# Performance work log

Measured on AMD Instinct MI355X. Metric: run time of the kernel, lower is better.

Reference implementation:

```python
import jax, jax.numpy as jnp
import numpy as np

B = 16384          # batch size
NUM_NEG = 4
N = 1 + NUM_NEG    # items per row (pos + negs)
D = 128            # embedding_dim
F = 4              # num_factors
FS = D // F        # factor_size = 32
TD = 384           # bert_text_dim
NU = 100000        # num_users
NI = 100000        # num_items
HID = 150          # text MLP hidden
M = 2              # num_modalities


def _linear_init(k, fan_out, fan_in):
    bound = 1.0 / np.sqrt(fan_in)
    return jax.random.uniform(k, (fan_out, fan_in), jnp.float32, -bound, bound)


def setup_inputs() -> dict:
    key = jax.random.key(0)
    ks = jax.random.split(key, 12)
    batch = jax.random.randint(ks[0], (B, 1 + N), 0, NU)          # col0=user, cols1..5=items
    text = jax.random.normal(ks[1], (B, N, TD), dtype=jnp.float32)
    user_table = jax.random.normal(ks[2], (NU, D), dtype=jnp.float32)
    item_table = jax.random.normal(ks[3], (NI, D), dtype=jnp.float32)
    w1 = _linear_init(ks[4], HID, TD)
    b1 = jax.random.uniform(ks[5], (HID,), jnp.float32, -1/np.sqrt(TD), 1/np.sqrt(TD))
    w2 = _linear_init(ks[6], D, HID)
    b2 = jax.random.uniform(ks[7], (D,), jnp.float32, -1/np.sqrt(HID), 1/np.sqrt(HID))
    # per-factor attention MLPs, stacked over the F factors (all same size here)
    aw1 = jax.random.uniform(ks[8], (F, M, 3 * FS), jnp.float32, -1/np.sqrt(3*FS), 1/np.sqrt(3*FS))
    ab1 = jax.random.uniform(ks[9], (F, M), jnp.float32, -1/np.sqrt(3*FS), 1/np.sqrt(3*FS))
    aw2 = jax.random.uniform(ks[10], (F, M, M), jnp.float32, -1/np.sqrt(M), 1/np.sqrt(M))
    return dict(batch=batch, text=text, user_table=user_table, item_table=item_table,
                w1=w1, b1=b1, w2=w2, b2=b2, aw1=aw1, ab1=ab1, aw2=aw2)


def _leaky_relu(x):
    return jnp.where(x > 0, x, 0.01 * x)


def reference(batch, text, user_table, item_table, w1, b1, w2, b2, aw1, ab1, aw2):
    # text MLP: Linear -> LeakyReLU -> Linear -> LeakyReLU
    te = _leaky_relu(_leaky_relu(text @ w1.T + b1) @ w2.T + b2)   # [B,N,D]

    users = batch[:, 0]
    items = batch[:, 1:]
    u = user_table[users]                                          # [B,D]
    ie = item_table[items]                                         # [B,N,D]

    # split into F factors of size FS (vectorized over factor dim)
    uf = jnp.broadcast_to(u[:, None, :], ie.shape).reshape(B, N, F, FS)
    itf = ie.reshape(B, N, F, FS)
    tf = te.reshape(B, N, F, FS)

    cat = jnp.concatenate([uf, itf, tf], axis=-1)                  # [B,N,F,3*FS]
    nrm = jnp.linalg.norm(cat, axis=-1, keepdims=True)
    cat = cat / jnp.maximum(nrm, 1e-12)                            # F.normalize(dim=-1)

    h = jnp.tanh(jnp.einsum('bnfk,fmk->bnfm', cat, aw1) + ab1)     # [B,N,F,M]
    logits = jnp.einsum('bnfm,fom->bnfo', h, aw2)                  # [B,N,F,M]
    # torch nn.Softmax() with dim=None on a 3D tensor -> softmax over dim 0 (batch)
    attn = jax.nn.softmax(logits, axis=0)

    r_ui = attn[..., 0] * jax.nn.softplus(jnp.sum(uf * itf, axis=-1))  # [B,N,F]
    r_ut = attn[..., 1] * jax.nn.softplus(jnp.sum(uf * tf, axis=-1))   # [B,N,F]
    ratings = jnp.sum(r_ui + r_ut, axis=-1)                        # [B,N], sum over factors
    return ratings
```

## Files before the change

### kernel.cpp

```cpp
#include <hip/hip_runtime.h>
#include <hip/hip_bf16.h>

#define TDIM 384
#define HID 150
#define DD 128
#define ROWS 81920
#define RT 32

typedef __attribute__((ext_vector_type(8))) short short8;
typedef __attribute__((ext_vector_type(4))) float f32x4;

#define SMEM_BYTES 16896

__device__ __forceinline__ float lrelu(float x) { return x > 0.f ? x : 0.01f * x; }
__device__ __forceinline__ float softplusf(float x) {
    return fmaxf(x, 0.f) + log1pf(expf(-fabsf(x)));
}

__device__ __forceinline__ short8 pack8(const float4 a, const float4 b) {
    union { short8 s; __hip_bfloat16 h[8]; } u;
    u.h[0] = __float2bfloat16(a.x); u.h[1] = __float2bfloat16(a.y);
    u.h[2] = __float2bfloat16(a.z); u.h[3] = __float2bfloat16(a.w);
    u.h[4] = __float2bfloat16(b.x); u.h[5] = __float2bfloat16(b.y);
    u.h[6] = __float2bfloat16(b.z); u.h[7] = __float2bfloat16(b.w);
    return u.s;
}

__global__ __launch_bounds__(256)
void prep_w(const float* __restrict__ w1, const float* __restrict__ w2,
            short8* __restrict__ w1f, short8* __restrict__ w2f)
{
    const int idx = blockIdx.x * 256 + threadIdx.x;
    union { short8 s; __hip_bfloat16 h[8]; } u;
    if (idx < 7680) {
        const int kt = idx / 640, c = idx % 640;
        const int col = c >> 2, q = c & 3;
        const int k = kt * 32 + q * 8;
#pragma unroll
        for (int j = 0; j < 8; ++j)
            u.h[j] = __float2bfloat16(col < HID ? w1[(size_t)col * TDIM + k + j] : 0.f);
        w1f[idx] = u.s;
    } else if (idx < 10240) {
        const int i2 = idx - 7680;
        const int kt = i2 / 512, c = i2 % 512;
        const int col = c >> 2, q = c & 3;
        const int k = kt * 32 + q * 8;
#pragma unroll
        for (int j = 0; j < 8; ++j)
            u.h[j] = __float2bfloat16((k + j) < HID ? w2[(size_t)col * HID + k + j] : 0.f);
        w2f[i2] = u.s;
    }
}

__global__ __launch_bounds__(256, 8)
void fused_main(const int* __restrict__ batch,
                const float* __restrict__ text,
                const float* __restrict__ user_table,
                const float* __restrict__ item_table,
                const short8* __restrict__ w1f,
                const float* __restrict__ b1,
                const short8* __restrict__ w2f,
                const float* __restrict__ b2,
                const float* __restrict__ aw1,
                const float* __restrict__ ab1,
                const float* __restrict__ aw2,
                float* __restrict__ expp,
                float* __restrict__ Sglob)
{
    __shared__ __align__(16) unsigned char smem[SMEM_BYTES];
    __shared__ __align__(8) float red[RT * 8];
    __hip_bfloat16* Hs = (__hip_bfloat16*)(smem);
    float*          Ts = (float*)(smem);

    const int t    = threadIdx.x;
    const int r0   = blockIdx.x * RT;
    const int lane = t & 63;
    const int wv   = t >> 6;
    const int m16  = lane & 15;
    const int quad = lane >> 4;
    const int wr   = (wv & 1) * 16;
    const int wc   = (wv >> 1) * 80;
    const int wc2  = (wv >> 1) * 64;

    const int p3row = t >> 3;
    const int p3f   = (t >> 1) & 3;
    const int half  = t & 1;
    const int gr    = r0 + p3row;
    const int bb    = gr / 5;
    const int nn    = gr - bb * 5;

    const float* ta  = text + (size_t)(r0 + wr + m16) * TDIM;
    const int    ko0 = quad * 8;
    const int w1base = (wc + m16) * 4 + quad;

    f32x4 acc1[5];
#pragma unroll
    for (int j = 0; j < 5; ++j) acc1[j] = (f32x4){0.f, 0.f, 0.f, 0.f};

    float4 pA[2][2];
#pragma unroll
    for (int k = 0; k < 2; ++k) {
        pA[k][0] = *(const float4*)(ta + k * 32 + ko0);
        pA[k][1] = *(const float4*)(ta + k * 32 + ko0 + 4);
    }

#pragma unroll
    for (int kt = 0; kt < 12; ++kt) {
        const int p = kt & 1;
        short8 bw[5];
#pragma unroll
        for (int tj = 0; tj < 5; ++tj)
            bw[tj] = w1f[kt * 640 + w1base + tj * 64];
        const short8 a0 = pack8(pA[p][0], pA[p][1]);
        if (kt < 10) {
            const int ko = (kt + 2) * 32 + ko0;
            pA[p][0] = *(const float4*)(ta + ko);
            pA[p][1] = *(const float4*)(ta + ko + 4);
        }
#pragma unroll
        for (int tj = 0; tj < 5; ++tj)
            acc1[tj] = __builtin_amdgcn_mfma_f32_16x16x32_bf16(a0, bw[tj], acc1[tj], 0, 0, 0);
    }

#pragma unroll
    for (int tj = 0; tj < 5; ++tj) {
        const int col = wc + tj * 16 + m16;
        const float bv = (col < HID) ? b1[col] : 0.f;
#pragma unroll
        for (int r = 0; r < 4; ++r) {
            const int row = wr + quad * 4 + r;
            float v = lrelu(acc1[tj][r] + bv);
            if (col >= HID) v = 0.f;
            Hs[row * 168 + col] = __float2bfloat16(v);
        }
    }
    __syncthreads();

    f32x4 acc2[4];
#pragma unroll
    for (int j = 0; j < 4; ++j) acc2[j] = (f32x4){0.f, 0.f, 0.f, 0.f};

    const __hip_bfloat16* h0p = Hs + (wr + m16) * 168 + ko0;
    const int w2base = (wc2 + m16) * 4 + quad;

#pragma unroll
    for (int kt = 0; kt < 5; ++kt) {
        short8 bw[4];
#pragma unroll
        for (int tj = 0; tj < 4; ++tj)
            bw[tj] = w2f[kt * 512 + w2base + tj * 64];
        const short8 a0 = *(const short8*)(h0p + kt * 32);
#pragma unroll
        for (int tj = 0; tj < 4; ++tj)
            acc2[tj] = __builtin_amdgcn_mfma_f32_16x16x32_bf16(a0, bw[tj], acc2[tj], 0, 0, 0);
    }
    __syncthreads();

#pragma unroll
    for (int tj = 0; tj < 4; ++tj) {
        const int col = wc2 + tj * 16 + m16;
        const float bv = b2[col];
#pragma unroll
        for (int r = 0; r < 4; ++r) {
            const int row = wr + quad * 4 + r;
            Ts[row * 132 + col] = lrelu(acc2[tj][r] + bv);
        }
    }

    const int uid = batch[bb * 6];
    const int iid = batch[bb * 6 + 1 + nn];
    const float* up = user_table + (size_t)uid * DD + p3f * 32 + half * 16;
    const float* ip = item_table + (size_t)iid * DD + p3f * 32 + half * 16;
    float4 ur[4], er[4];
#pragma unroll
    for (int q = 0; q < 4; ++q) {
        ur[q] = *(const float4*)(up + q * 4);
        er[q] = *(const float4*)(ip + q * 4);
    }
    __syncthreads();

    {
        const float* tp  = Ts + p3row * 132 + p3f * 32 + half * 16;
        const float* a1p = aw1 + p3f * 192 + half * 16;

        float ss = 0.f, z0 = 0.f, z1 = 0.f, sui = 0.f, sut = 0.f;
#pragma unroll
        for (int q = 0; q < 4; ++q) {
            const float4 u4 = ur[q];
            const float4 e4 = er[q];
            const float4 t4 = *(const float4*)(tp + q * 4);
            const float4 a00 = *(const float4*)(a1p + q * 4);
            const float4 a01 = *(const float4*)(a1p + 32 + q * 4);
            const float4 a02 = *(const float4*)(a1p + 64 + q * 4);
            const float4 a10 = *(const float4*)(a1p + 96 + q * 4);
            const float4 a11 = *(const float4*)(a1p + 128 + q * 4);
            const float4 a12 = *(const float4*)(a1p + 160 + q * 4);
            const float uu[4] = {u4.x, u4.y, u4.z, u4.w};
            const float ee[4] = {e4.x, e4.y, e4.z, e4.w};
            const float tt[4] = {t4.x, t4.y, t4.z, t4.w};
            const float w00[4] = {a00.x, a00.y, a00.z, a00.w};
            const float w01[4] = {a01.x, a01.y, a01.z, a01.w};
            const float w02[4] = {a02.x, a02.y, a02.z, a02.w};
            const float w10[4] = {a10.x, a10.y, a10.z, a10.w};
            const float w11[4] = {a11.x, a11.y, a11.z, a11.w};
            const float w12[4] = {a12.x, a12.y, a12.z, a12.w};
#pragma unroll
            for (int c = 0; c < 4; ++c) {
                const float u = uu[c], e = ee[c], x = tt[c];
                ss  = fmaf(u, u, ss); ss = fmaf(e, e, ss); ss = fmaf(x, x, ss);
                z0  = fmaf(u, w00[c], z0);
                z0  = fmaf(e, w01[c], z0);
                z0  = fmaf(x, w02[c], z0);
                z1  = fmaf(u, w10[c], z1);
                z1  = fmaf(e, w11[c], z1);
                z1  = fmaf(x, w12[c], z1);
                sui = fmaf(u, e, sui);
                sut = fmaf(u, x, sut);
            }
        }
        ss  += __shfl_xor(ss, 1);
        z0  += __shfl_xor(z0, 1);
        z1  += __shfl_xor(z1, 1);
        sui += __shfl_xor(sui, 1);
        sut += __shfl_xor(sut, 1);

        const float inv = 1.f / fmaxf(sqrtf(ss), 1e-12f);
        const float h0 = tanhf(fmaf(z0, inv, ab1[p3f * 2 + 0]));
        const float h1 = tanhf(fmaf(z1, inv, ab1[p3f * 2 + 1]));
        const float l0 = fmaf(h0, aw2[p3f * 4 + 0], h1 * aw2[p3f * 4 + 1]);
        const float l1 = fmaf(h0, aw2[p3f * 4 + 2], h1 * aw2[p3f * 4 + 3]);
        const float e0 = expf(l0), e1 = expf(l1);
        const float pui = softplusf(sui), put = softplusf(sut);
        if (half == 0) {
            *(float4*)&expp[((size_t)gr * 4 + p3f) * 4] = make_float4(e0, e1, pui, put);
            *(float2*)&red[p3row * 8 + p3f * 2] = make_float2(e0, e1);
        }
    }
    __syncthreads();

    if (t < 40) {
        const int j   = t & 7;
        const int nn0 = t >> 3;
        const int rep = blockIdx.x & 7;
        int r = nn0 - (r0 % 5);
        if (r < 0) r += 5;
        float s = 0.f;
        for (; r < RT; r += 5) s += red[r * 8 + j];
        atomicAdd(&Sglob[((t * 8) + rep) * 16], s);
    }
}

__global__ __launch_bounds__(256)
void finalize(const float* __restrict__ expp,
              const float* __restrict__ Sglob,
              float* __restrict__ out)
{
    __shared__ float Ss[40];
    const int t = threadIdx.x;

    if (t < 160) {
        const int cidx = t >> 2;
        const int rp   = t & 3;
        float v = Sglob[(cidx * 8 + rp * 2 + 0) * 16]
                + Sglob[(cidx * 8 + rp * 2 + 1) * 16];
        v += __shfl_xor(v, 1);
        v += __shfl_xor(v, 2);
        if (rp == 0) Ss[cidx] = v;
    }
    __syncthreads();

    const int gr = blockIdx.x * 256 + t;
    const int b = gr / 5;
    const int n = gr - b * 5;
    float r = 0.f;
#pragma unroll
    for (int f = 0; f < 4; ++f) {
        const float4 v = *(const float4*)&expp[((size_t)gr * 4 + f) * 4];
        const float S0 = Ss[n * 8 + f * 2 + 0];
        const float S1 = Ss[n * 8 + f * 2 + 1];
        r += v.x / S0 * v.z + v.y / S1 * v.w;
    }
    out[gr] = r;
}

extern "C" void kernel_launch(void* const* d_in, const int* in_sizes, int n_in,
                              void* d_out, int out_size, void* d_ws, size_t ws_size,
                              hipStream_t stream)
{
    (void)in_sizes; (void)n_in; (void)out_size; (void)ws_size;
    const int*   batch      = (const int*)d_in[0];
    const float* text       = (const float*)d_in[1];
    const float* user_table = (const float*)d_in[2];
    const float* item_table = (const float*)d_in[3];
    const float* w1         = (const float*)d_in[4];
    const float* b1         = (const float*)d_in[5];
    const float* w2         = (const float*)d_in[6];
    const float* b2         = (const float*)d_in[7];
    const float* aw1        = (const float*)d_in[8];
    const float* ab1        = (const float*)d_in[9];
    const float* aw2        = (const float*)d_in[10];
    float* out = (float*)d_out;

    char* ws = (char*)d_ws;
    short8* w1f   = (short8*)ws;
    short8* w2f   = (short8*)(ws + 122880);
    float*  expp  = (float*)(ws + 163840);
    float*  Sglob = (float*)(ws + 163840 + (size_t)ROWS * 16 * 4);

    hipMemsetAsync(Sglob, 0, 320 * 16 * sizeof(float), stream);
    prep_w<<<40, 256, 0, stream>>>(w1, w2, w1f, w2f);
    fused_main<<<ROWS / RT, 256, 0, stream>>>(batch, text, user_table, item_table,
                                              w1f, b1, w2f, b2, aw1, ab1, aw2,
                                              expp, Sglob);
    finalize<<<ROWS / 256, 256, 0, stream>>>(expp, Sglob, out);
}
```

Baseline: 334.6 us.

## Double-buffer weight fragments, hoist embedding gathers, stage aw1 in LDS

Weight fragments for both MLP GEMM loops are now double-buffered in registers, so the next k-step's weights load while the current MFMAs run. The user and item embedding gathers move up to just after the first GEMM, so their latency overlaps the second GEMM. The attention weights aw1 are copied into padded shared memory and read from there instead of global memory. The reduction buffer is folded into the same shared allocation. The extra registers and shared memory lower the occupancy hint from 8 to 6 blocks, which may reduce latency hiding.

```diff
diff --git a/kernel.cpp b/kernel.cpp
--- a/kernel.cpp
+++ b/kernel.cpp
@@ -10,7 +10,7 @@
 typedef __attribute__((ext_vector_type(8))) short short8;
 typedef __attribute__((ext_vector_type(4))) float f32x4;
 
-#define SMEM_BYTES 16896
+#define SMEM_BYTES 21120
 
 __device__ __forceinline__ float lrelu(float x) { return x > 0.f ? x : 0.01f * x; }
 __device__ __forceinline__ float softplusf(float x) {
@@ -52,7 +52,7 @@
     }
 }
 
-__global__ __launch_bounds__(256, 8)
+__global__ __launch_bounds__(256, 6)
 void fused_main(const int* __restrict__ batch,
                 const float* __restrict__ text,
                 const float* __restrict__ user_table,
@@ -68,9 +68,10 @@
                 float* __restrict__ Sglob)
 {
     __shared__ __align__(16) unsigned char smem[SMEM_BYTES];
-    __shared__ __align__(8) float red[RT * 8];
-    __hip_bfloat16* Hs = (__hip_bfloat16*)(smem);
-    float*          Ts = (float*)(smem);
+    __hip_bfloat16* Hs   = (__hip_bfloat16*)(smem);
+    float*          Ts   = (float*)(smem);
+    float*          aw1L = (float*)(smem + 16896);
+    float*          redL = (float*)(smem + 20096);
 
     const int t    = threadIdx.x;
     const int r0   = blockIdx.x * RT;
@@ -89,6 +90,11 @@
     const int bb    = gr / 5;
     const int nn    = gr - bb * 5;
 
+    if (t < 192) {
+        const int f = t / 48, j = t % 48;
+        *(float4*)&aw1L[f * 200 + j * 4] = *(const float4*)&aw1[f * 192 + j * 4];
+    }
+
     const float* ta  = text + (size_t)(r0 + wr + m16) * TDIM;
     const int    ko0 = quad * 8;
     const int w1base = (wc + m16) * 4 + quad;
@@ -103,24 +109,65 @@
         pA[k][0] = *(const float4*)(ta + k * 32 + ko0);
         pA[k][1] = *(const float4*)(ta + k * 32 + ko0 + 4);
     }
-
-#pragma unroll
-    for (int kt = 0; kt < 12; ++kt) {
-        const int p = kt & 1;
-        short8 bw[5];
-#pragma unroll
-        for (int tj = 0; tj < 5; ++tj)
-            bw[tj] = w1f[kt * 640 + w1base + tj * 64];
-        const short8 a0 = pack8(pA[p][0], pA[p][1]);
-        if (kt < 10) {
-            const int ko = (kt + 2) * 32 + ko0;
-            pA[p][0] = *(const float4*)(ta + ko);
-            pA[p][1] = *(const float4*)(ta + ko + 4);
-        }
-#pragma unroll
-        for (int tj = 0; tj < 5; ++tj)
-            acc1[tj] = __builtin_amdgcn_mfma_f32_16x16x32_bf16(a0, bw[tj], acc1[tj], 0, 0, 0);
-    }
+    short8 bw0[5], bw1[5];
+#pragma unroll
+    for (int tj = 0; tj < 5; ++tj) bw0[tj] = w1f[w1base + tj * 64];
+#pragma unroll
+    for (int tj = 0; tj < 5; ++tj) bw1[tj] = w1f[640 + w1base + tj * 64];
+
+#pragma unroll
+    for (int kt = 0; kt < 12; kt += 2) {
+        {
+            const short8 a0 = pack8(pA[0][0], pA[0][1]);
+            if (kt < 10) {
+                const int ko = (kt + 2) * 32 + ko0;
+                pA[0][0] = *(const float4*)(ta + ko);
+                pA[0][1] = *(const float4*)(ta + ko + 4);
+            }
+#pragma unroll
+            for (int tj = 0; tj < 5; ++tj)
+                acc1[tj] = __builtin_amdgcn_mfma_f32_16x16x32_bf16(a0, bw0[tj], acc1[tj], 0, 0, 0);
+            if (kt < 10) {
+#pragma unroll
+                for (int tj = 0; tj < 5; ++tj)
+                    bw0[tj] = w1f[(kt + 2) * 640 + w1base + tj * 64];
+            }
+        }
+        {
+            const short8 a1 = pack8(pA[1][0], pA[1][1]);
+            if (kt < 10) {
+                const int ko = (kt + 3) * 32 + ko0;
+                pA[1][0] = *(const float4*)(ta + ko);
+                pA[1][1] = *(const float4*)(ta + ko + 4);
+            }
+#pragma unroll
+            for (int tj = 0; tj < 5; ++tj)
+                acc1[tj] = __builtin_amdgcn_mfma_f32_16x16x32_bf16(a1, bw1[tj], acc1[tj], 0, 0, 0);
+            if (kt < 10) {
+#pragma unroll
+                for (int tj = 0; tj < 5; ++tj)
+                    bw1[tj] = w1f[(kt + 3) * 640 + w1base + tj * 64];
+            }
+        }
+    }
+
+    const int uid = batch[bb * 6];
+    const int iid = batch[bb * 6 + 1 + nn];
+    const float* up = user_table + (size_t)uid * DD + p3f * 32 + half * 16;
+    const float* ip = item_table + (size_t)iid * DD + p3f * 32 + half * 16;
+    float4 ur[4], er[4];
+#pragma unroll
+    for (int q = 0; q < 4; ++q) {
+        ur[q] = *(const float4*)(up + q * 4);
+        er[q] = *(const float4*)(ip + q * 4);
+    }
+
+    const int w2base = (wc2 + m16) * 4 + quad;
+    short8 c0[4], c1[4];
+#pragma unroll
+    for (int tj = 0; tj < 4; ++tj) c0[tj] = w2f[w2base + tj * 64];
+#pragma unroll
+    for (int tj = 0; tj < 4; ++tj) c1[tj] = w2f[512 + w2base + tj * 64];
 
 #pragma unroll
     for (int tj = 0; tj < 5; ++tj) {
@@ -141,18 +188,42 @@
     for (int j = 0; j < 4; ++j) acc2[j] = (f32x4){0.f, 0.f, 0.f, 0.f};
 
     const __hip_bfloat16* h0p = Hs + (wr + m16) * 168 + ko0;
-    const int w2base = (wc2 + m16) * 4 + quad;
-
-#pragma unroll
-    for (int kt = 0; kt < 5; ++kt) {
-        short8 bw[4];
-#pragma unroll
-        for (int tj = 0; tj < 4; ++tj)
-            bw[tj] = w2f[kt * 512 + w2base + tj * 64];
-        const short8 a0 = *(const short8*)(h0p + kt * 32);
-#pragma unroll
-        for (int tj = 0; tj < 4; ++tj)
-            acc2[tj] = __builtin_amdgcn_mfma_f32_16x16x32_bf16(a0, bw[tj], acc2[tj], 0, 0, 0);
+
+    {
+        const short8 a0 = *(const short8*)(h0p + 0 * 32);
+#pragma unroll
+        for (int tj = 0; tj < 4; ++tj)
+            acc2[tj] = __builtin_amdgcn_mfma_f32_16x16x32_bf16(a0, c0[tj], acc2[tj], 0, 0, 0);
+#pragma unroll
+        for (int tj = 0; tj < 4; ++tj) c0[tj] = w2f[2 * 512 + w2base + tj * 64];
+    }
+    {
+        const short8 a0 = *(const short8*)(h0p + 1 * 32);
+#pragma unroll
+        for (int tj = 0; tj < 4; ++tj)
+            acc2[tj] = __builtin_amdgcn_mfma_f32_16x16x32_bf16(a0, c1[tj], acc2[tj], 0, 0, 0);
+#pragma unroll
+        for (int tj = 0; tj < 4; ++tj) c1[tj] = w2f[3 * 512 + w2base + tj * 64];
+    }
+    {
+        const short8 a0 = *(const short8*)(h0p + 2 * 32);
+#pragma unroll
+        for (int tj = 0; tj < 4; ++tj)
+            acc2[tj] = __builtin_amdgcn_mfma_f32_16x16x32_bf16(a0, c0[tj], acc2[tj], 0, 0, 0);
+#pragma unroll
+        for (int tj = 0; tj < 4; ++tj) c0[tj] = w2f[4 * 512 + w2base + tj * 64];
+    }
+    {
+        const short8 a0 = *(const short8*)(h0p + 3 * 32);
+#pragma unroll
+        for (int tj = 0; tj < 4; ++tj)
+            acc2[tj] = __builtin_amdgcn_mfma_f32_16x16x32_bf16(a0, c1[tj], acc2[tj], 0, 0, 0);
+    }
+    {
+        const short8 a0 = *(const short8*)(h0p + 4 * 32);
+#pragma unroll
+        for (int tj = 0; tj < 4; ++tj)
+            acc2[tj] = __builtin_amdgcn_mfma_f32_16x16x32_bf16(a0, c0[tj], acc2[tj], 0, 0, 0);
     }
     __syncthreads();
 
@@ -166,22 +237,11 @@
             Ts[row * 132 + col] = lrelu(acc2[tj][r] + bv);
         }
     }
-
-    const int uid = batch[bb * 6];
-    const int iid = batch[bb * 6 + 1 + nn];
-    const float* up = user_table + (size_t)uid * DD + p3f * 32 + half * 16;
-    const float* ip = item_table + (size_t)iid * DD + p3f * 32 + half * 16;
-    float4 ur[4], er[4];
-#pragma unroll
-    for (int q = 0; q < 4; ++q) {
-        ur[q] = *(const float4*)(up + q * 4);
-        er[q] = *(const float4*)(ip + q * 4);
-    }
     __syncthreads();
 
     {
         const float* tp  = Ts + p3row * 132 + p3f * 32 + half * 16;
-        const float* a1p = aw1 + p3f * 192 + half * 16;
+        const float* a1p = aw1L + p3f * 200 + half * 16;
 
         float ss = 0.f, z0 = 0.f, z1 = 0.f, sui = 0.f, sut = 0.f;
 #pragma unroll
@@ -233,7 +293,7 @@
         const float pui = softplusf(sui), put = softplusf(sut);
         if (half == 0) {
             *(float4*)&expp[((size_t)gr * 4 + p3f) * 4] = make_float4(e0, e1, pui, put);
-            *(float2*)&red[p3row * 8 + p3f * 2] = make_float2(e0, e1);
+            *(float2*)&redL[p3row * 8 + p3f * 2] = make_float2(e0, e1);
         }
     }
     __syncthreads();
@@ -245,7 +305,7 @@
         int r = nn0 - (r0 % 5);
         if (r < 0) r += 5;
         float s = 0.f;
-        for (; r < RT; r += 5) s += red[r * 8 + j];
+        for (; r < RT; r += 5) s += redL[r * 8 + j];
         atomicAdd(&Sglob[((t * 8) + rep) * 16], s);
     }
 }
```

New measurement: 338.6 us. No clear change (+1.2%).
